# Performance work log

Hardware: AMD Instinct MI355X
Metric: run time of the kernel (lower is better)

## Reference

```python
import jax, jax.numpy as jnp
import numpy as np

NPOINT = 512
RADIUS = 0.2
NSAMPLE = 32
EPS = 1e-5  # BatchNorm eps


def _fps(x, npoint):
    """Farthest point sampling. x: [B,N,3] -> idx [B,npoint] int32.
    Deterministic start at index 0 (original uses a random start index)."""
    B, N, _ = x.shape

    def step(carry, _):
        dist, far = carry
        c = jnp.take_along_axis(x, far[:, None, None], axis=1)  # [B,1,3]
        d = jnp.sum((x - c) ** 2, axis=-1)                      # [B,N]
        dist = jnp.minimum(dist, d)
        return (dist, jnp.argmax(dist, axis=-1).astype(jnp.int32)), far

    init = (jnp.full((B, N), 1e10, x.dtype), jnp.zeros((B,), jnp.int32))
    _, cent = jax.lax.scan(step, init, None, length=npoint)  # [npoint,B]
    return cent.T


def _gather(pts, idx):
    # pts: [B,N,C], idx: [B,...] -> [B,...,C]
    return jax.vmap(lambda a, i: a[i])(pts, idx)


def _sqdist(a, b):
    # a: [B,S,3], b: [B,N,3] -> [B,S,N]  (same expansion as square_distance)
    return (jnp.sum(a ** 2, -1, keepdims=True)
            + jnp.sum(b ** 2, -1)[:, None, :]
            - 2.0 * jnp.einsum('bsc,bnc->bsn', a, b))


def _bn_relu(h, g, be):
    # training-mode BatchNorm over (B,S,K), channel-last h: [B,S,K,C]
    m = jnp.mean(h, axis=(0, 1, 2))
    v = jnp.var(h, axis=(0, 1, 2))
    return jax.nn.relu((h - m) * jax.lax.rsqrt(v + EPS) * g + be)


def _forward(xyz, points, params):
    x = jnp.transpose(xyz, (0, 2, 1))     # [B,N,3]
    p = jnp.transpose(points, (0, 2, 1))  # [B,N,D]
    B, N, _ = x.shape

    fps_idx = _fps(x, NPOINT)             # [B,S]
    new_xyz = _gather(x, fps_idx)         # [B,S,3]

    # ball query: keep indices within radius, sort, take first NSAMPLE,
    # pad misses with the first valid index (same as torch code)
    sqr = _sqdist(new_xyz, x)             # [B,S,N]
    gi = jnp.where(sqr <= RADIUS * RADIUS, jnp.arange(N)[None, None, :], N)
    gi = jnp.sort(gi, axis=-1)[:, :, :NSAMPLE]  # [B,S,K]
    gi = jnp.where(gi == N, gi[:, :, :1], gi)

    grouped_xyz = _gather(x, gi) - new_xyz[:, :, None, :]  # [B,S,K,3]
    grouped_p = _gather(p, gi)                             # [B,S,K,D]
    h = jnp.concatenate([grouped_xyz, grouped_p], axis=-1)  # [B,S,K,3+D]

    for (W, b, g, be) in params:  # shared 1x1 conv == per-point linear
        h = _bn_relu(jnp.einsum('bskc,oc->bsko', h, W) + b, g, be)

    new_points = jnp.transpose(jnp.max(h, axis=2), (0, 2, 1))  # [B,C_out,S]
    return jnp.transpose(new_xyz, (0, 2, 1)), new_points       # [B,3,S], [B,C,S]


def setup_inputs() -> dict:
    key = jax.random.key(0)
    ks = jax.random.split(key, 10)
    B, N, D = 16, 4096, 3
    inp = {
        'xyz': jax.random.uniform(ks[0], (B, 3, N), jnp.float32),
        'points': jax.random.uniform(ks[1], (B, D, N), jnp.float32),
    }
    dims = [(6, 64), (64, 64), (64, 128)]
    for i, (cin, cout) in enumerate(dims):
        inp[f'W{i}'] = jax.random.normal(ks[2 + 2 * i], (cout, cin), jnp.float32) * 0.1
        inp[f'b{i}'] = jax.random.normal(ks[3 + 2 * i], (cout,), jnp.float32) * 0.1
        inp[f'g{i}'] = jnp.ones((cout,), jnp.float32)
        inp[f'be{i}'] = jnp.zeros((cout,), jnp.float32)
    return inp


def reference(xyz, points, W0, b0, g0, be0, W1, b1, g1, be1, W2, b2, g2, be2):
    params = [(W0, b0, g0, be0), (W1, b1, g1, be1), (W2, b2, g2, be2)]
    return _forward(xyz, points, params)
```

## Files before the change

### kernel.cpp

```cpp
#include <hip/hip_runtime.h>
#include <hip/hip_bf16.h>

#define BB 16
#define NN 4096
#define SS 512
#define KK 32
#define CNTF 262144.0f
#define FT 256
#define FP 16

typedef short bf16x8 __attribute__((ext_vector_type(8)));
typedef float f32x4 __attribute__((ext_vector_type(4)));

__device__ __forceinline__ unsigned short f2bf(float x) {
  __hip_bfloat16 h = __float2bfloat16(x);
  return *reinterpret_cast<unsigned short*>(&h);
}

#define DPP_COMBINE(kk, CTRL)                                                         \
  {                                                                                   \
    unsigned lo_ = (unsigned)(kk), hi_ = (unsigned)((kk) >> 32);                      \
    unsigned plo_ = (unsigned)__builtin_amdgcn_update_dpp(0, (int)lo_, (CTRL), 0xF, 0xF, true); \
    unsigned phi_ = (unsigned)__builtin_amdgcn_update_dpp(0, (int)hi_, (CTRL), 0xF, 0xF, true); \
    unsigned long long ok_ = ((unsigned long long)phi_ << 32) | plo_;                 \
    kk = (kk) > ok_ ? (kk) : ok_;                                                     \
  }

__global__ __launch_bounds__(FT) void k_fps(const float* __restrict__ xyz,
                                            float* __restrict__ newxyz,
                                            float* __restrict__ dout) {
  __shared__ __align__(16) float4 ps[NN];
  __shared__ __align__(16) unsigned long long sKey[2][4];
  const int b = blockIdx.x;
  const int tid = threadIdx.x;
  const int wid = tid >> 6;
  const float* px = xyz + (size_t)b * 3 * NN;
  float lx[FP], ly[FP], lz[FP], dist[FP];
#pragma unroll
  for (int j = 0; j < FP; j++) {
    int n = j * FT + tid;
    float x = px[n], y = px[NN + n], z = px[2 * NN + n];
    lx[j] = x; ly[j] = y; lz[j] = z;
    ps[n] = make_float4(x, y, z, 0.f);
    dist[j] = 1e10f;
  }
  __syncthreads();
  float cx = px[0], cy = px[NN], cz = px[2 * NN];
  float c0x = 0.f, c0y = 0.f, c0z = 0.f, c1x = 0.f, c1y = 0.f, c1z = 0.f;
  for (int s = 0;; s++) {
    bool cap = (tid == (s & 255));
    if (s < 256) {
      if (cap) { c0x = cx; c0y = cy; c0z = cz; }
    } else {
      if (cap) { c1x = cx; c1y = cy; c1z = cz; }
    }
    if (s == SS - 1) break;
    float bestd = -1.0f;
    unsigned bestn = 0u;
#pragma unroll
    for (int j = 0; j < FP; j++) {
      float dx = __fsub_rn(lx[j], cx);
      float dy = __fsub_rn(ly[j], cy);
      float dz = __fsub_rn(lz[j], cz);
      float d = __fadd_rn(__fadd_rn(__fmul_rn(dx, dx), __fmul_rn(dy, dy)), __fmul_rn(dz, dz));
      float dm = fminf(dist[j], d);
      dist[j] = dm;
      if (dm > bestd) { bestd = dm; bestn = (unsigned)(j * FT + tid); }
    }
    unsigned long long wbest =
        ((unsigned long long)__float_as_uint(bestd) << 32) | (unsigned)(~bestn);
    DPP_COMBINE(wbest, 0xB1);
    DPP_COMBINE(wbest, 0x4E);
    DPP_COMBINE(wbest, 0x141);
    DPP_COMBINE(wbest, 0x140);
    DPP_COMBINE(wbest, 0x142);
    DPP_COMBINE(wbest, 0x143);
    int p = s & 1;
    if ((tid & 63) == 63) sKey[p][wid] = wbest;
    __syncthreads();
    const ulonglong2* kp = (const ulonglong2*)&sKey[p][0];
    ulonglong2 v0 = kp[0], v1 = kp[1];
    unsigned long long ka = (v0.y > v0.x) ? v0.y : v0.x;
    unsigned long long kb = (v1.y > v1.x) ? v1.y : v1.x;
    unsigned long long km = (kb > ka) ? kb : ka;
    unsigned n = ~(unsigned)km;
    float4 c4 = ps[n];
    cx = c4.x; cy = c4.y; cz = c4.z;
  }
  {
    float* nx0 = newxyz + ((size_t)b * SS + tid) * 3;
    nx0[0] = c0x; nx0[1] = c0y; nx0[2] = c0z;
    float* nx1 = newxyz + ((size_t)b * SS + 256 + tid) * 3;
    nx1[0] = c1x; nx1[1] = c1y; nx1[2] = c1z;
    float* d0 = dout + (size_t)b * 3 * SS;
    d0[tid] = c0x;        d0[SS + tid] = c0y;        d0[2 * SS + tid] = c0z;
    d0[256 + tid] = c1x;  d0[SS + 256 + tid] = c1y;  d0[2 * SS + 256 + tid] = c1z;
  }
}

__global__ __launch_bounds__(256) void k_ball(const float* __restrict__ xyz,
                                              const float* __restrict__ newxyz,
                                              int* __restrict__ gi) {
  const int lane = threadIdx.x & 63;
  const int w = threadIdx.x >> 6;
  const int idx = blockIdx.x * 4 + w;
  const int b = idx >> 9;
  const float* px = xyz + (size_t)b * 3 * NN;
  const float* c = newxyz + (size_t)idx * 3;
  const double R2 = 0.2 * 0.2;
  double cx = (double)c[0], cy = (double)c[1], cz = (double)c[2];
  double ca = cx * cx + cy * cy + cz * cz;
  int total = 0;
  int first_n = 0;
  bool found = false;
  unsigned long long lt = (1ull << lane) - 1ull;
  for (int chunk = 0; chunk < NN / 64; chunk++) {
    int n = chunk * 64 + lane;
    double x = (double)px[n], y = (double)px[NN + n], z = (double)px[2 * NN + n];
    double sb = x * x + y * y + z * z;
    double dot = cx * x + cy * y + cz * z;
    double sqr = (ca + sb) - 2.0 * dot;
    bool in = sqr <= R2;
    unsigned long long m = __ballot(in);
    if (!found && m) { first_n = chunk * 64 + __builtin_ctzll(m); found = true; }
    int rank = total + __popcll(m & lt);
    if (in && rank < KK) gi[(size_t)idx * KK + rank] = n;
    total += __popcll(m);
    if (total >= KK) break;
  }
  if (total < KK) {
    for (int slot = total + lane; slot < KK; slot += 64) gi[(size_t)idx * KK + slot] = first_n;
  }
}

__global__ __launch_bounds__(256) void k_group_stats(const float* __restrict__ xyz,
                                                     const float* __restrict__ pts,
                                                     const float* __restrict__ newxyz,
                                                     const int* __restrict__ gi,
                                                     const float* __restrict__ W0,
                                                     const float* __restrict__ b0,
                                                     float* __restrict__ h0,
                                                     float* __restrict__ part) {
  __shared__ float hs[256 * 6];
  __shared__ float sred[512];
  int tid = threadIdx.x;
  int base = blockIdx.x * 256;
  int m = base + tid;
  int b = m >> 14;
  int bs = m >> 5;
  int n = gi[m];
  const float* px = xyz + (size_t)b * 3 * NN;
  const float* pp = pts + (size_t)b * 3 * NN;
  const float* c = newxyz + (size_t)bs * 3;
  float f0 = px[n] - c[0];
  float f1 = px[NN + n] - c[1];
  float f2 = px[2 * NN + n] - c[2];
  float f3 = pp[n];
  float f4 = pp[NN + n];
  float f5 = pp[2 * NN + n];
  float* o = h0 + (size_t)m * 6;
  o[0] = f0; o[1] = f1; o[2] = f2; o[3] = f3; o[4] = f4; o[5] = f5;
  float* hr = hs + tid * 6;
  hr[0] = f0; hr[1] = f1; hr[2] = f2; hr[3] = f3; hr[4] = f4; hr[5] = f5;
  __syncthreads();
  int cc = tid & 63, g = tid >> 6;
  float w[6];
#pragma unroll
  for (int j = 0; j < 6; j++) w[j] = W0[cc * 6 + j];
  float bb = b0[cc];
  float s1 = 0.f, s2 = 0.f;
  for (int i = g; i < 256; i += 4) {
    float v = bb;
#pragma unroll
    for (int j = 0; j < 6; j++) v = fmaf(w[j], hs[i * 6 + j], v);
    s1 += v; s2 = fmaf(v, v, s2);
  }
  sred[tid] = s1; sred[256 + tid] = s2;
  __syncthreads();
  if (tid < 64) {
    float a = 0.f, q = 0.f;
#pragma unroll
    for (int g2 = 0; g2 < 4; g2++) { a += sred[tid + 64 * g2]; q += sred[256 + tid + 64 * g2]; }
    part[blockIdx.x * 256 + tid] = a;
    part[blockIdx.x * 256 + 128 + tid] = q;
  }
}

__global__ __launch_bounds__(256) void k_reduce(const float* __restrict__ part, int NBLK,
                                                const float* __restrict__ gamma,
                                                const float* __restrict__ beta,
                                                float* __restrict__ scale,
                                                float* __restrict__ shift) {
  __shared__ float sr[512];
  int c = blockIdx.x;
  int tid = threadIdx.x;
  float s1 = 0.f, s2 = 0.f;
  for (int nb = tid; nb < NBLK; nb += 256) {
    s1 += part[(size_t)nb * 256 + c];
    s2 += part[(size_t)nb * 256 + 128 + c];
  }
  sr[tid] = s1; sr[256 + tid] = s2;
  __syncthreads();
  for (int off = 128; off >= 1; off >>= 1) {
    if (tid < off) { sr[tid] += sr[tid + off]; sr[256 + tid] += sr[256 + tid + off]; }
    __syncthreads();
  }
  if (tid == 0) {
    float m = sr[0] / CNTF;
    float v = sr[256] / CNTF - m * m;
    float sc = gamma[c] / sqrtf(v + 1e-5f);
    scale[c] = sc;
    shift[c] = beta[c] - m * sc;
  }
}

__global__ __launch_bounds__(256) void k_l2(const float* __restrict__ h0,
                                            const float* __restrict__ W0,
                                            const float* __restrict__ b0,
                                            const float* __restrict__ scale1,
                                            const float* __restrict__ shift1,
                                            const float* __restrict__ W1,
                                            const float* __restrict__ b1,
                                            __hip_bfloat16* __restrict__ l2,
                                            float* __restrict__ part) {
  __shared__ float hs[128 * 6];
  __shared__ __align__(16) unsigned short a1s[128][64];
  __shared__ __align__(16) unsigned short w1s[64][64];
  __shared__ float sst1[64][17];
  __shared__ float sst2[64][17];
  __shared__ float sb1[64];
  int tid = threadIdx.x;
  int base = blockIdx.x * 128;
  for (int t = tid; t < 768; t += 256) hs[t] = h0[(size_t)base * 6 + t];
  for (int t = tid; t < 4096; t += 256) {
    int n = t >> 6, k = t & 63;
    int kc = (k >> 3) ^ (n & 7);
    w1s[n][kc * 8 + (k & 7)] = f2bf(W1[t]);
  }
  if (tid < 64) sb1[tid] = b1[tid];
  __syncthreads();
  for (int t = tid; t < 8192; t += 256) {
    int i = t >> 6, k = t & 63;
    float v = b0[k];
#pragma unroll
    for (int j = 0; j < 6; j++) v = fmaf(W0[k * 6 + j], hs[i * 6 + j], v);
    float a = fmaxf(fmaf(scale1[k], v, shift1[k]), 0.f);
    int kc = (k >> 3) ^ (i & 7);
    a1s[i][kc * 8 + (k & 7)] = f2bf(a);
  }
  __syncthreads();
  int w = tid >> 6, l = tid & 63, lr = l & 15, lk = l >> 4;
  bf16x8 A[2][2];
#pragma unroll
  for (int mt = 0; mt < 2; mt++) {
    int row = (w * 2 + mt) * 16 + lr;
#pragma unroll
    for (int kb = 0; kb < 2; kb++) {
      int kc = (kb * 4 + lk) ^ (row & 7);
      A[mt][kb] = *(const bf16x8*)&a1s[row][kc * 8];
    }
  }
  f32x4 acc[2][4];
#pragma unroll
  for (int mt = 0; mt < 2; mt++)
#pragma unroll
    for (int nt = 0; nt < 4; nt++) acc[mt][nt] = f32x4{0.f, 0.f, 0.f, 0.f};
#pragma unroll
  for (int nt = 0; nt < 4; nt++) {
    int n = nt * 16 + lr;
    int kc0 = lk ^ (n & 7);
    int kc1 = (4 + lk) ^ (n & 7);
    bf16x8 B0 = *(const bf16x8*)&w1s[n][kc0 * 8];
    bf16x8 B1 = *(const bf16x8*)&w1s[n][kc1 * 8];
#pragma unroll
    for (int mt = 0; mt < 2; mt++) {
      acc[mt][nt] = __builtin_amdgcn_mfma_f32_16x16x32_bf16(A[mt][0], B0, acc[mt][nt], 0, 0, 0);
      acc[mt][nt] = __builtin_amdgcn_mfma_f32_16x16x32_bf16(A[mt][1], B1, acc[mt][nt], 0, 0, 0);
    }
  }
  int slot = w * 4 + lk;
#pragma unroll
  for (int nt = 0; nt < 4; nt++) {
    int cch = nt * 16 + lr;
    float bias = sb1[cch];
    float s1 = 0.f, s2 = 0.f;
#pragma unroll
    for (int mt = 0; mt < 2; mt++)
#pragma unroll
      for (int r = 0; r < 4; r++) {
        float v = acc[mt][nt][r] + bias;
        int row = (w * 2 + mt) * 16 + lk * 4 + r;
        l2[(size_t)(base + row) * 64 + cch] = __float2bfloat16(v);
        s1 += v; s2 = fmaf(v, v, s2);
      }
    sst1[cch][slot] = s1; sst2[cch][slot] = s2;
  }
  __syncthreads();
  if (tid < 64) {
    float s1 = 0.f, s2 = 0.f;
#pragma unroll
    for (int t = 0; t < 16; t++) { s1 += sst1[tid][t]; s2 += sst2[tid][t]; }
    part[blockIdx.x * 256 + tid] = s1;
    part[blockIdx.x * 256 + 128 + tid] = s2;
  }
}

__global__ __launch_bounds__(256) void k_l3pass(const __hip_bfloat16* __restrict__ l2,
                                                const float* __restrict__ scale2,
                                                const float* __restrict__ shift2,
                                                const float* __restrict__ W2,
                                                const float* __restrict__ b2,
                                                float* __restrict__ part,
                                                float* __restrict__ pmax) {
  __shared__ __align__(16) unsigned short a2s[128][64];
  __shared__ __align__(16) unsigned short w2s[128][64];
  __shared__ float sst1[128][17];
  __shared__ float sst2[128][17];
  __shared__ float smx[128][17];
  __shared__ float sb2[128];
  int tid = threadIdx.x;
  size_t base = (size_t)blockIdx.x * 128;
  for (int t = tid; t < 8192; t += 256) {
    int i = t >> 6, k = t & 63;
    float v = __bfloat162float(l2[base * 64 + t]);
    float a = fmaxf(fmaf(scale2[k], v, shift2[k]), 0.f);
    int kc = (k >> 3) ^ (i & 7);
    a2s[i][kc * 8 + (k & 7)] = f2bf(a);
  }
  for (int t = tid; t < 8192; t += 256) {
    int n = t >> 6, k = t & 63;
    int kc = (k >> 3) ^ (n & 7);
    w2s[n][kc * 8 + (k & 7)] = f2bf(W2[t]);
  }
  if (tid < 128) sb2[tid] = b2[tid];
  __syncthreads();
  int w = tid >> 6, l = tid & 63, lr = l & 15, lk = l >> 4;
  bf16x8 A[2][2];
#pragma unroll
  for (int mt = 0; mt < 2; mt++) {
    int row = (w * 2 + mt) * 16 + lr;
#pragma unroll
    for (int kb = 0; kb < 2; kb++) {
      int kc = (kb * 4 + lk) ^ (row & 7);
      A[mt][kb] = *(const bf16x8*)&a2s[row][kc * 8];
    }
  }
  f32x4 acc[2][8];
#pragma unroll
  for (int mt = 0; mt < 2; mt++)
#pragma unroll
    for (int nt = 0; nt < 8; nt++) acc[mt][nt] = f32x4{0.f, 0.f, 0.f, 0.f};
#pragma unroll
  for (int nt = 0; nt < 8; nt++) {
    int n = nt * 16 + lr;
    int kc0 = lk ^ (n & 7);
    int kc1 = (4 + lk) ^ (n & 7);
    bf16x8 B0 = *(const bf16x8*)&w2s[n][kc0 * 8];
    bf16x8 B1 = *(const bf16x8*)&w2s[n][kc1 * 8];
#pragma unroll
    for (int mt = 0; mt < 2; mt++) {
      acc[mt][nt] = __builtin_amdgcn_mfma_f32_16x16x32_bf16(A[mt][0], B0, acc[mt][nt], 0, 0, 0);
      acc[mt][nt] = __builtin_amdgcn_mfma_f32_16x16x32_bf16(A[mt][1], B1, acc[mt][nt], 0, 0, 0);
    }
  }
  int slot = w * 4 + lk;
#pragma unroll
  for (int nt = 0; nt < 8; nt++) {
    int c = nt * 16 + lr;
    float bias = sb2[c];
    float s1 = 0.f, s2 = 0.f, mx = -3.4e38f;
#pragma unroll
    for (int mt = 0; mt < 2; mt++)
#pragma unroll
      for (int r = 0; r < 4; r++) {
        float v = acc[mt][nt][r] + bias;
        s1 += v; s2 = fmaf(v, v, s2); mx = fmaxf(mx, v);
      }
    sst1[c][slot] = s1; sst2[c][slot] = s2; smx[c][slot] = mx;
  }
  __syncthreads();
  if (tid < 128) {
    int c = tid;
    float s1 = 0.f, s2 = 0.f;
#pragma unroll
    for (int t = 0; t < 16; t++) { s1 += sst1[c][t]; s2 += sst2[c][t]; }
    part[blockIdx.x * 256 + c] = s1;
    part[blockIdx.x * 256 + 128 + c] = s2;
#pragma unroll
    for (int q = 0; q < 4; q++) {
      float m = fmaxf(fmaxf(smx[c][4 * q + 0], smx[c][4 * q + 1]),
                      fmaxf(smx[c][4 * q + 2], smx[c][4 * q + 3]));
      pmax[((size_t)blockIdx.x * 4 + q) * 128 + c] = m;
    }
  }
}

__global__ __launch_bounds__(256) void k_bn3(const float* __restrict__ pmax,
                                             const float* __restrict__ scale3,
                                             const float* __restrict__ shift3,
                                             float* __restrict__ dout) {
  __shared__ float tile[32][129];
  int tid = threadIdx.x;
  int b = blockIdx.x >> 4;
  int s0 = (blockIdx.x & 15) * 32;
  const float* src = pmax + ((size_t)b * SS + s0) * 128;
  for (int t = tid; t < 4096; t += 256) {
    int r = t >> 7, c = t & 127;
    tile[r][c] = src[r * 128 + c];
  }
  __syncthreads();
  float* dst = dout + 24576 + (size_t)b * 128 * SS;
  for (int t = tid; t < 4096; t += 256) {
    int c = t >> 5, r = t & 31;
    float v = tile[r][c];
    dst[(size_t)c * SS + s0 + r] = fmaxf(fmaf(scale3[c], v, shift3[c]), 0.f);
  }
}

extern "C" void kernel_launch(void* const* d_in, const int* in_sizes, int n_in,
                              void* d_out, int out_size, void* d_ws, size_t ws_size,
                              hipStream_t stream) {
  const float* xyz = (const float*)d_in[0];
  const float* pts = (const float*)d_in[1];
  const float* W0 = (const float*)d_in[2];
  const float* b0 = (const float*)d_in[3];
  const float* g0 = (const float*)d_in[4];
  const float* be0 = (const float*)d_in[5];
  const float* W1 = (const float*)d_in[6];
  const float* b1 = (const float*)d_in[7];
  const float* g1 = (const float*)d_in[8];
  const float* be1 = (const float*)d_in[9];
  const float* W2 = (const float*)d_in[10];
  const float* b2 = (const float*)d_in[11];
  const float* g2 = (const float*)d_in[12];
  const float* be2 = (const float*)d_in[13];
  float* out = (float*)d_out;

  char* ws = (char*)d_ws;
  int* gi = (int*)(ws + 32768);
  float* newxyz = (float*)(ws + 1081344);
  float* h0 = (float*)(ws + 1179648);
  float* pmax = h0;
  float* part = (float*)(ws + 7471104);
  float* scale1 = (float*)(ws + 9568256);
  float* shift1 = scale1 + 128;
  float* scale2 = shift1 + 128;
  float* shift2 = scale2 + 128;
  float* scale3 = shift2 + 128;
  float* shift3 = scale3 + 128;
  __hip_bfloat16* l2 = (__hip_bfloat16*)(ws + 9571328);

  k_fps<<<BB, FT, 0, stream>>>(xyz, newxyz, out);
  k_ball<<<2048, 256, 0, stream>>>(xyz, newxyz, gi);
  k_group_stats<<<1024, 256, 0, stream>>>(xyz, pts, newxyz, gi, W0, b0, h0, part);
  k_reduce<<<64, 256, 0, stream>>>(part, 1024, g0, be0, scale1, shift1);
  k_l2<<<2048, 256, 0, stream>>>(h0, W0, b0, scale1, shift1, W1, b1, l2, part);
  k_reduce<<<64, 256, 0, stream>>>(part, 2048, g1, be1, scale2, shift2);
  k_l3pass<<<2048, 256, 0, stream>>>(l2, scale2, shift2, W2, b2, part, pmax);
  k_reduce<<<128, 256, 0, stream>>>(part, 2048, g2, be2, scale3, shift3);
  k_bn3<<<256, 256, 0, stream>>>(pmax, scale3, shift3, out);
}
```

Measured before the change: 426.9 us.

## Replace BatchNorm reduce kernels with atomic stat accumulation and in-kernel finalize

```diff
diff --git a/kernel.cpp b/kernel.cpp
--- a/kernel.cpp
+++ b/kernel.cpp
@@ -26,14 +26,19 @@
     kk = (kk) > ok_ ? (kk) : ok_;                                                     \
   }
 
+
 __global__ __launch_bounds__(FT) void k_fps(const float* __restrict__ xyz,
                                             float* __restrict__ newxyz,
-                                            float* __restrict__ dout) {
+                                            float* __restrict__ dout,
+                                            float* __restrict__ stats) {
   __shared__ __align__(16) float4 ps[NN];
   __shared__ __align__(16) unsigned long long sKey[2][4];
   const int b = blockIdx.x;
   const int tid = threadIdx.x;
   const int wid = tid >> 6;
+  if (b == 0) {
+    for (int t = tid; t < 768; t += FT) stats[t] = 0.f;
+  }
   const float* px = xyz + (size_t)b * 3 * NN;
   float lx[FP], ly[FP], lz[FP], dist[FP];
 #pragma unroll
@@ -140,7 +145,7 @@
                                                      const float* __restrict__ W0,
                                                      const float* __restrict__ b0,
                                                      float* __restrict__ h0,
-                                                     float* __restrict__ part) {
+                                                     float* __restrict__ stats) {
   __shared__ float hs[256 * 6];
   __shared__ float sred[512];
   int tid = threadIdx.x;
@@ -181,54 +186,27 @@
     float a = 0.f, q = 0.f;
 #pragma unroll
     for (int g2 = 0; g2 < 4; g2++) { a += sred[tid + 64 * g2]; q += sred[256 + tid + 64 * g2]; }
-    part[blockIdx.x * 256 + tid] = a;
-    part[blockIdx.x * 256 + 128 + tid] = q;
-  }
-}
-
-__global__ __launch_bounds__(256) void k_reduce(const float* __restrict__ part, int NBLK,
-                                                const float* __restrict__ gamma,
-                                                const float* __restrict__ beta,
-                                                float* __restrict__ scale,
-                                                float* __restrict__ shift) {
-  __shared__ float sr[512];
-  int c = blockIdx.x;
-  int tid = threadIdx.x;
-  float s1 = 0.f, s2 = 0.f;
-  for (int nb = tid; nb < NBLK; nb += 256) {
-    s1 += part[(size_t)nb * 256 + c];
-    s2 += part[(size_t)nb * 256 + 128 + c];
-  }
-  sr[tid] = s1; sr[256 + tid] = s2;
-  __syncthreads();
-  for (int off = 128; off >= 1; off >>= 1) {
-    if (tid < off) { sr[tid] += sr[tid + off]; sr[256 + tid] += sr[256 + tid + off]; }
-    __syncthreads();
-  }
-  if (tid == 0) {
-    float m = sr[0] / CNTF;
-    float v = sr[256] / CNTF - m * m;
-    float sc = gamma[c] / sqrtf(v + 1e-5f);
-    scale[c] = sc;
-    shift[c] = beta[c] - m * sc;
+    atomicAdd(&stats[tid], a);
+    atomicAdd(&stats[128 + tid], q);
   }
 }
 
 __global__ __launch_bounds__(256) void k_l2(const float* __restrict__ h0,
                                             const float* __restrict__ W0,
                                             const float* __restrict__ b0,
-                                            const float* __restrict__ scale1,
-                                            const float* __restrict__ shift1,
+                                            const float* __restrict__ g0,
+                                            const float* __restrict__ be0,
+                                            float* __restrict__ stats,
                                             const float* __restrict__ W1,
                                             const float* __restrict__ b1,
-                                            __hip_bfloat16* __restrict__ l2,
-                                            float* __restrict__ part) {
+                                            __hip_bfloat16* __restrict__ l2) {
   __shared__ float hs[128 * 6];
   __shared__ __align__(16) unsigned short a1s[128][64];
   __shared__ __align__(16) unsigned short w1s[64][64];
   __shared__ float sst1[64][17];
   __shared__ float sst2[64][17];
   __shared__ float sb1[64];
+  __shared__ float ssc1[64], ssh1[64];
   int tid = threadIdx.x;
   int base = blockIdx.x * 128;
   for (int t = tid; t < 768; t += 256) hs[t] = h0[(size_t)base * 6 + t];
@@ -237,14 +215,22 @@
     int kc = (k >> 3) ^ (n & 7);
     w1s[n][kc * 8 + (k & 7)] = f2bf(W1[t]);
   }
-  if (tid < 64) sb1[tid] = b1[tid];
+  if (tid < 64) {
+    sb1[tid] = b1[tid];
+    float sm = stats[tid], sq = stats[128 + tid];
+    float mm = sm / CNTF;
+    float vv = sq / CNTF - mm * mm;
+    float sc = g0[tid] / sqrtf(vv + 1e-5f);
+    ssc1[tid] = sc;
+    ssh1[tid] = be0[tid] - mm * sc;
+  }
   __syncthreads();
   for (int t = tid; t < 8192; t += 256) {
     int i = t >> 6, k = t & 63;
     float v = b0[k];
 #pragma unroll
     for (int j = 0; j < 6; j++) v = fmaf(W0[k * 6 + j], hs[i * 6 + j], v);
-    float a = fmaxf(fmaf(scale1[k], v, shift1[k]), 0.f);
+    float a = fmaxf(fmaf(ssc1[k], v, ssh1[k]), 0.f);
     int kc = (k >> 3) ^ (i & 7);
     a1s[i][kc * 8 + (k & 7)] = f2bf(a);
   }
@@ -300,17 +286,17 @@
     float s1 = 0.f, s2 = 0.f;
 #pragma unroll
     for (int t = 0; t < 16; t++) { s1 += sst1[tid][t]; s2 += sst2[tid][t]; }
-    part[blockIdx.x * 256 + tid] = s1;
-    part[blockIdx.x * 256 + 128 + tid] = s2;
+    atomicAdd(&stats[256 + tid], s1);
+    atomicAdd(&stats[384 + tid], s2);
   }
 }
 
 __global__ __launch_bounds__(256) void k_l3pass(const __hip_bfloat16* __restrict__ l2,
-                                                const float* __restrict__ scale2,
-                                                const float* __restrict__ shift2,
+                                                const float* __restrict__ g1,
+                                                const float* __restrict__ be1,
+                                                float* __restrict__ stats,
                                                 const float* __restrict__ W2,
                                                 const float* __restrict__ b2,
-                                                float* __restrict__ part,
                                                 float* __restrict__ pmax) {
   __shared__ __align__(16) unsigned short a2s[128][64];
   __shared__ __align__(16) unsigned short w2s[128][64];
@@ -318,21 +304,31 @@
   __shared__ float sst2[128][17];
   __shared__ float smx[128][17];
   __shared__ float sb2[128];
+  __shared__ float ssc2[64], ssh2[64];
   int tid = threadIdx.x;
   size_t base = (size_t)blockIdx.x * 128;
-  for (int t = tid; t < 8192; t += 256) {
-    int i = t >> 6, k = t & 63;
-    float v = __bfloat162float(l2[base * 64 + t]);
-    float a = fmaxf(fmaf(scale2[k], v, shift2[k]), 0.f);
-    int kc = (k >> 3) ^ (i & 7);
-    a2s[i][kc * 8 + (k & 7)] = f2bf(a);
-  }
+  if (tid < 64) {
+    float sm = stats[256 + tid], sq = stats[384 + tid];
+    float mm = sm / CNTF;
+    float vv = sq / CNTF - mm * mm;
+    float sc = g1[tid] / sqrtf(vv + 1e-5f);
+    ssc2[tid] = sc;
+    ssh2[tid] = be1[tid] - mm * sc;
+  }
+  if (tid < 128) sb2[tid] = b2[tid];
   for (int t = tid; t < 8192; t += 256) {
     int n = t >> 6, k = t & 63;
     int kc = (k >> 3) ^ (n & 7);
     w2s[n][kc * 8 + (k & 7)] = f2bf(W2[t]);
   }
-  if (tid < 128) sb2[tid] = b2[tid];
+  __syncthreads();
+  for (int t = tid; t < 8192; t += 256) {
+    int i = t >> 6, k = t & 63;
+    float v = __bfloat162float(l2[base * 64 + t]);
+    float a = fmaxf(fmaf(ssc2[k], v, ssh2[k]), 0.f);
+    int kc = (k >> 3) ^ (i & 7);
+    a2s[i][kc * 8 + (k & 7)] = f2bf(a);
+  }
   __syncthreads();
   int w = tid >> 6, l = tid & 63, lr = l & 15, lk = l >> 4;
   bf16x8 A[2][2];
@@ -384,8 +380,8 @@
     float s1 = 0.f, s2 = 0.f;
 #pragma unroll
     for (int t = 0; t < 16; t++) { s1 += sst1[c][t]; s2 += sst2[c][t]; }
-    part[blockIdx.x * 256 + c] = s1;
-    part[blockIdx.x * 256 + 128 + c] = s2;
+    atomicAdd(&stats[512 + c], s1);
+    atomicAdd(&stats[640 + c], s2);
 #pragma unroll
     for (int q = 0; q < 4; q++) {
       float m = fmaxf(fmaxf(smx[c][4 * q + 0], smx[c][4 * q + 1]),
@@ -396,13 +392,23 @@
 }
 
 __global__ __launch_bounds__(256) void k_bn3(const float* __restrict__ pmax,
-                                             const float* __restrict__ scale3,
-                                             const float* __restrict__ shift3,
+                                             const float* __restrict__ g2,
+                                             const float* __restrict__ be2,
+                                             const float* __restrict__ stats,
                                              float* __restrict__ dout) {
   __shared__ float tile[32][129];
+  __shared__ float ssc3[128], ssh3[128];
   int tid = threadIdx.x;
   int b = blockIdx.x >> 4;
   int s0 = (blockIdx.x & 15) * 32;
+  if (tid < 128) {
+    float sm = stats[512 + tid], sq = stats[640 + tid];
+    float mm = sm / CNTF;
+    float vv = sq / CNTF - mm * mm;
+    float sc = g2[tid] / sqrtf(vv + 1e-5f);
+    ssc3[tid] = sc;
+    ssh3[tid] = be2[tid] - mm * sc;
+  }
   const float* src = pmax + ((size_t)b * SS + s0) * 128;
   for (int t = tid; t < 4096; t += 256) {
     int r = t >> 7, c = t & 127;
@@ -413,7 +419,7 @@
   for (int t = tid; t < 4096; t += 256) {
     int c = t >> 5, r = t & 31;
     float v = tile[r][c];
-    dst[(size_t)c * SS + s0 + r] = fmaxf(fmaf(scale3[c], v, shift3[c]), 0.f);
+    dst[(size_t)c * SS + s0 + r] = fmaxf(fmaf(ssc3[c], v, ssh3[c]), 0.f);
   }
 }
 
@@ -441,22 +447,13 @@
   float* newxyz = (float*)(ws + 1081344);
   float* h0 = (float*)(ws + 1179648);
   float* pmax = h0;
-  float* part = (float*)(ws + 7471104);
-  float* scale1 = (float*)(ws + 9568256);
-  float* shift1 = scale1 + 128;
-  float* scale2 = shift1 + 128;
-  float* shift2 = scale2 + 128;
-  float* scale3 = shift2 + 128;
-  float* shift3 = scale3 + 128;
+  float* stats = (float*)(ws + 7471104);
   __hip_bfloat16* l2 = (__hip_bfloat16*)(ws + 9571328);
 
-  k_fps<<<BB, FT, 0, stream>>>(xyz, newxyz, out);
+  k_fps<<<BB, FT, 0, stream>>>(xyz, newxyz, out, stats);
   k_ball<<<2048, 256, 0, stream>>>(xyz, newxyz, gi);
-  k_group_stats<<<1024, 256, 0, stream>>>(xyz, pts, newxyz, gi, W0, b0, h0, part);
-  k_reduce<<<64, 256, 0, stream>>>(part, 1024, g0, be0, scale1, shift1);
-  k_l2<<<2048, 256, 0, stream>>>(h0, W0, b0, scale1, shift1, W1, b1, l2, part);
-  k_reduce<<<64, 256, 0, stream>>>(part, 2048, g1, be1, scale2, shift2);
-  k_l3pass<<<2048, 256, 0, stream>>>(l2, scale2, shift2, W2, b2, part, pmax);
-  k_reduce<<<128, 256, 0, stream>>>(part, 2048, g2, be2, scale3, shift3);
-  k_bn3<<<256, 256, 0, stream>>>(pmax, scale3, shift3, out);
-}
+  k_group_stats<<<1024, 256, 0, stream>>>(xyz, pts, newxyz, gi, W0, b0, h0, stats);
+  k_l2<<<2048, 256, 0, stream>>>(h0, W0, b0, g0, be0, stats, W1, b1, l2);
+  k_l3pass<<<2048, 256, 0, stream>>>(l2, g1, be1, stats, W2, b2, pmax);
+  k_bn3<<<256, 256, 0, stream>>>(pmax, g2, be2, stats, out);
+}
```

After: 502.4 us. 1.18x slower.
